# Kernel optimization log

Measured on AMD Instinct MI355X. Metric: run time of the kernel, lower is better.

Reference implementation:

```python
import jax, jax.numpy as jnp
import numpy as np
import math

B, S, D, H = 4, 2048, 1024, 16
DH = D // H
NEG = -1e10


def setup_inputs() -> dict:
    key = jax.random.key(0)
    k1, k2, k3 = jax.random.split(key, 3)
    x = jax.random.normal(k1, (B, S, D), dtype=jnp.float32)
    # torch nn.Linear weights have shape (out_features, in_features); y = x @ W.T + b
    w1 = jax.random.normal(k2, (3 * D, D), dtype=jnp.float32) * (1.0 / math.sqrt(D))
    b1 = jnp.zeros((3 * D,), dtype=jnp.float32)
    w2 = jax.random.normal(k3, (D, D), dtype=jnp.float32) * (1.0 / math.sqrt(D))
    b2 = jnp.zeros((D,), dtype=jnp.float32)
    return {"x": x, "w1": w1, "b1": b1, "w2": w2, "b2": b2}


def reference(x, w1, b1, w2, b2):
    b, s, d = x.shape
    h, dh = H, d // H
    qkv = x @ w1.T + b1                                  # [B,S,3D]
    q, k, v = jnp.split(qkv, 3, axis=-1)                 # each [B,S,D]
    def heads(t):
        return t.reshape(b, s, h, dh).transpose(0, 2, 1, 3)  # [B,H,S,dh]
    q, k, v = heads(q), heads(k), heads(v)
    # additive causal mask: (1 - tril) * -1e10, as in the original
    mask = (1.0 - jnp.tril(jnp.ones((s, s), dtype=x.dtype))) * NEG
    scores = jnp.einsum('bhqd,bhkd->bhqk', q, k) / math.sqrt(dh) + mask
    attn = jax.nn.softmax(scores, axis=-1)
    o = jnp.einsum('bhqk,bhkd->bhqd', attn, v)           # [B,H,S,dh]
    o = o.transpose(0, 2, 1, 3).reshape(b, s, d)         # [B,S,D]
    return o @ w2.T + b2
```

## Files before the change

kernel.cpp:

```cpp
#include <hip/hip_runtime.h>
#include <stdint.h>


typedef __bf16 bf16;
typedef __attribute__((ext_vector_type(4))) __bf16 bf16x4;
typedef __attribute__((ext_vector_type(8))) __bf16 bf16x8;
typedef __attribute__((ext_vector_type(4))) float f32x4;
typedef __attribute__((ext_vector_type(16))) float f32x16;

#define MFMA16(a, b, c) __builtin_amdgcn_mfma_f32_16x16x32_bf16((a), (b), (c), 0, 0, 0)
#define MFMA32(a, b, c) __builtin_amdgcn_mfma_f32_32x32x16_bf16((a), (b), (c), 0, 0, 0)

#if __has_builtin(__builtin_amdgcn_exp2f)
#define EXP2F(x) __builtin_amdgcn_exp2f(x)
#else
#define EXP2F(x) exp2f(x)
#endif

#define GLOAD_LDS16(gp, lp)                                                    \
  __builtin_amdgcn_global_load_lds(                                            \
      (__attribute__((address_space(1))) void*)(gp),                           \
      (__attribute__((address_space(3))) void*)(lp), 16, 0, 0)

#define SB   2048
#define D3   3072
#define DD   1024
#define QSCALE 0.18033688011112042f

__global__ __launch_bounds__(256) void cast_bf16_kernel(
    const float* __restrict__ in, bf16* __restrict__ out, int n4) {
  int stride = gridDim.x * blockDim.x;
  for (int i = blockIdx.x * blockDim.x + threadIdx.x; i < n4; i += stride) {
    float4 v = ((const float4*)in)[i];
    bf16x4 p;
    p[0] = (bf16)v.x; p[1] = (bf16)v.y; p[2] = (bf16)v.z; p[3] = (bf16)v.w;
    *(bf16x4*)(out + (size_t)i * 4) = p;
  }
}

template <int OUTMODE>
__global__ __launch_bounds__(256, 2) void gemm2p_kernel(
    const bf16* __restrict__ A, const bf16* __restrict__ Bw,
    const float* __restrict__ bias, void* __restrict__ Cout,
    int M, int N, int K, int NBn) {
  __shared__ __attribute__((aligned(16))) bf16 As[2][128 * 64];
  __shared__ __attribute__((aligned(16))) bf16 Bs[2][128 * 64];
  const int tid = threadIdx.x;
  const int w = tid >> 6, l = tid & 63;
  const int lr = l & 31, lh = l >> 5;
  const int wm = w >> 1, wn = w & 1;
  const int nwg = gridDim.x;
  const int sw = ((int)blockIdx.x % 8) * (nwg / 8) + (int)blockIdx.x / 8;
  const int bn = sw % NBn, bm = sw / NBn;
  const int m0 = bm * 128, n0 = bn * 128;
  const int NT = K >> 6;

  const int srow = l >> 3;
  const int scol = ((l & 7) ^ srow) << 3;

  auto stage = [&](int buf, int kt) {
#pragma unroll
    for (int j = 0; j < 4; ++j) {
      const int rb = j * 32 + w * 8 + srow;
      GLOAD_LDS16(A + (size_t)(m0 + rb) * K + kt * 64 + scol,
                  (char*)&As[buf][0] + j * 4096 + w * 1024);
      GLOAD_LDS16(Bw + (size_t)(n0 + rb) * K + kt * 64 + scol,
                  (char*)&Bs[buf][0] + j * 4096 + w * 1024);
    }
  };

  auto ldA = [&](int buf, int ks, bf16x8 (&aF)[2]) {
#pragma unroll
    for (int ti = 0; ti < 2; ++ti) {
      const int r = wm * 64 + ti * 32 + lr;
      aF[ti] = *(const bf16x8*)((const char*)&As[buf][0] + r * 128 +
                                (((ks * 2 + lh) ^ (lr & 7)) << 4));
    }
  };
  auto ldB = [&](int buf, int ks, bf16x8 (&bF)[2]) {
#pragma unroll
    for (int tj = 0; tj < 2; ++tj) {
      const int r = wn * 64 + tj * 32 + lr;
      bF[tj] = *(const bf16x8*)((const char*)&Bs[buf][0] + r * 128 +
                                (((ks * 2 + lh) ^ (lr & 7)) << 4));
    }
  };

  f32x16 acc[2][2] = {};
  auto domfma = [&](bf16x8 (&aF)[2], bf16x8 (&bF)[2]) {
    __builtin_amdgcn_s_setprio(1);
#pragma unroll
    for (int ti = 0; ti < 2; ++ti)
#pragma unroll
      for (int tj = 0; tj < 2; ++tj)
        acc[ti][tj] = MFMA32(aF[ti], bF[tj], acc[ti][tj]);
    __builtin_amdgcn_s_setprio(0);
  };

  stage(0, 0);
  __syncthreads();

  for (int T = 0; T < NT; ++T) {
    const int buf = T & 1;
    if (T + 1 < NT) stage(buf ^ 1, T + 1);
    bf16x8 aP[2], bP[2], aQ[2], bQ[2];
    ldA(buf, 0, aP); ldB(buf, 0, bP);
    ldA(buf, 1, aQ); ldB(buf, 1, bQ); domfma(aP, bP);
    ldA(buf, 2, aP); ldB(buf, 2, bP); domfma(aQ, bQ);
    ldA(buf, 3, aQ); ldB(buf, 3, bQ); domfma(aP, bP);
    domfma(aQ, bQ);
    __syncthreads();
  }

#pragma unroll
  for (int ti = 0; ti < 2; ++ti) {
    const int r0 = m0 + wm * 64 + ti * 32 + 4 * lh;
#pragma unroll
    for (int tj = 0; tj < 2; ++tj) {
      const int col = n0 + wn * 64 + tj * 32 + lr;
      const float bv = bias[col];
#pragma unroll
      for (int e = 0; e < 16; ++e) {
        const int row = r0 + (e & 3) + 8 * (e >> 2);
        float v = acc[ti][tj][e] + bv;
        if (OUTMODE == 1) {
          if (col < DD) v *= QSCALE;
          ((bf16*)Cout)[(size_t)row * N + col] = (bf16)v;
        } else {
          ((float*)Cout)[(size_t)row * N + col] = v;
        }
      }
    }
  }
}

__global__ __launch_bounds__(256) void vtrans_kernel(
    const bf16* __restrict__ qkv, bf16* __restrict__ vT) {
  __shared__ __attribute__((aligned(16))) bf16 tt[64 * 72];
  const int tid = threadIdx.x;
  const int bh = blockIdx.x >> 5, st = blockIdx.x & 31;
  const int b = bh >> 4, h = bh & 15;
  const int s0 = st * 64;
  const int sr = tid >> 3, c0 = (tid & 7) * 8;
#pragma unroll
  for (int i = 0; i < 2; ++i) {
    const int srr = sr + i * 32;
    bf16x8 v = *(const bf16x8*)(qkv + (size_t)(b * SB + s0 + srr) * D3 + 2 * DD + h * 64 + c0);
    *(bf16x8*)(&tt[srr * 72 + c0]) = v;
  }
  __syncthreads();
  const int d = tid >> 2;
#pragma unroll
  for (int i = 0; i < 2; ++i) {
    const int sc = (tid & 3) * 2 + i;
    bf16x8 v;
#pragma unroll
    for (int j = 0; j < 8; ++j) v[j] = tt[(sc * 8 + j) * 72 + d];
    *(bf16x8*)(vT + (size_t)(bh * 64 + d) * SB + s0 + sc * 8) = v;
  }
}

__global__ __launch_bounds__(256, 2) void attn_kernel(
    const bf16* __restrict__ qkv, const bf16* __restrict__ vT,
    bf16* __restrict__ o) {
  __shared__ __attribute__((aligned(16))) bf16 Kt[2][128 * 64];
  __shared__ __attribute__((aligned(16))) bf16 Vt[2][64 * 128];
  const int tid = threadIdx.x;
  const int w = tid >> 6, l = tid & 63;
  const int c = l & 15, g = l >> 4;
  const int pair = blockIdx.x >> 6, bh = blockIdx.x & 63;
  const int b = bh >> 4, h = bh & 15;
  const int qtA = pair, qtB = 15 - pair;
  const int swz = (c & 7) << 4;

  const bf16* qg = qkv + (size_t)(b * SB) * D3 + h * 64;

  auto stage = [&](int kt, int buf) {
#pragma unroll
    for (int j = 0; j < 4; ++j) {
      const int row = w * 32 + j * 8 + (l >> 3);
      const int cs = ((l & 7) ^ (row & 7)) << 3;
      GLOAD_LDS16(qkv + (size_t)(b * SB + kt * 128 + row) * D3 + DD + h * 64 + cs,
                  (char*)&Kt[buf][0] + w * 4096 + j * 1024);
    }
#pragma unroll
    for (int j = 0; j < 4; ++j) {
      const int row = w * 16 + j * 4 + (l >> 4);
      const int cs = ((l & 15) ^ (row & 7)) << 3;
      GLOAD_LDS16(vT + (size_t)(bh * 64 + row) * SB + kt * 128 + cs,
                  (char*)&Vt[buf][0] + w * 4096 + j * 1024);
    }
  };

  stage(0, 0);

  bf16x8 qfA[2][2], qfB[2][2];
#pragma unroll
  for (int mi = 0; mi < 2; ++mi)
#pragma unroll
    for (int dk = 0; dk < 2; ++dk) {
      qfA[mi][dk] = *(const bf16x8*)(qg + (size_t)(qtA * 128 + w * 32 + mi * 16 + c) * D3 + dk * 32 + g * 8);
      qfB[mi][dk] = *(const bf16x8*)(qg + (size_t)(qtB * 128 + w * 32 + mi * 16 + c) * D3 + dk * 32 + g * 8);
    }

  f32x4 ofA[2][4] = {}, ofB[2][4] = {};
  float mA[2] = {-1e30f, -1e30f}, lA[2] = {0.f, 0.f};
  float mB[2] = {-1e30f, -1e30f}, lB[2] = {0.f, 0.f};
  const f32x4 zero = {0.f, 0.f, 0.f, 0.f};

  auto process = [&](int kt, int qt, int buf, bf16x8 (&qf)[2][2], float (&m)[2],
                     float (&lsum)[2], f32x4 (&of)[2][4]) {
    f32x4 sf[2][8];
#pragma unroll
    for (int f = 0; f < 8; ++f) {
      const char* kr = (const char*)&Kt[buf][0] + (f * 16 + c) * 128;
      bf16x8 kb0 = *(const bf16x8*)(kr + ((g * 16) ^ swz));
      bf16x8 kb1 = *(const bf16x8*)(kr + ((64 + g * 16) ^ swz));
#pragma unroll
      for (int mi = 0; mi < 2; ++mi) {
        f32x4 t = MFMA16(kb0, qf[mi][0], zero);
        sf[mi][f] = MFMA16(kb1, qf[mi][1], t);
      }
    }

    if (kt == qt) {
#pragma unroll
      for (int mi = 0; mi < 2; ++mi) {
        const int qloc = w * 32 + mi * 16 + c;
#pragma unroll
        for (int f = 0; f < 8; ++f)
#pragma unroll
          for (int r = 0; r < 4; ++r)
            if (f * 16 + 4 * g + r > qloc) sf[mi][f][r] = -1e30f;
      }
    }

    bf16x8 pa[2][4];
#pragma unroll
    for (int mi = 0; mi < 2; ++mi) {
      float pm = -1e30f;
#pragma unroll
      for (int f = 0; f < 8; ++f)
#pragma unroll
        for (int r = 0; r < 4; ++r) pm = fmaxf(pm, sf[mi][f][r]);
      pm = fmaxf(pm, __shfl_xor(pm, 16, 64));
      pm = fmaxf(pm, __shfl_xor(pm, 32, 64));
      if (__any(pm > m[mi] + 8.f)) {
        const float mnew = fmaxf(m[mi], pm);
        const float sc = EXP2F(m[mi] - mnew);
        m[mi] = mnew;
        lsum[mi] *= sc;
#pragma unroll
        for (int di = 0; di < 4; ++di) of[mi][di] *= sc;
      }
      float rs = 0.f;
#pragma unroll
      for (int f = 0; f < 8; ++f)
#pragma unroll
        for (int r = 0; r < 4; ++r) {
          const float pv = EXP2F(sf[mi][f][r] - m[mi]);
          sf[mi][f][r] = pv;
          rs += pv;
        }
      rs += __shfl_xor(rs, 16, 64);
      rs += __shfl_xor(rs, 32, 64);
      lsum[mi] += rs;
#pragma unroll
      for (int t = 0; t < 4; ++t)
#pragma unroll
        for (int s = 0; s < 4; ++s) {
          pa[mi][t][s]     = (bf16)sf[mi][2 * t][s];
          pa[mi][t][4 + s] = (bf16)sf[mi][2 * t + 1][s];
        }
    }

#pragma unroll
    for (int di = 0; di < 4; ++di) {
      const char* vrow = (const char*)&Vt[buf][0] + (di * 16 + c) * 256;
#pragma unroll
      for (int t = 0; t < 4; ++t) {
        bf16x4 v1 = *(const bf16x4*)(vrow + ((64 * t + 8 * g) ^ swz));
        bf16x4 v2 = *(const bf16x4*)(vrow + ((64 * t + 32 + 8 * g) ^ swz));
        bf16x8 va;
#pragma unroll
        for (int s = 0; s < 4; ++s) { va[s] = v1[s]; va[4 + s] = v2[s]; }
#pragma unroll
        for (int mi = 0; mi < 2; ++mi)
          of[mi][di] = MFMA16(va, pa[mi][t], of[mi][di]);
      }
    }
  };

  __syncthreads();

  int buf = 0;
  for (int kt = 0; kt <= qtB; ++kt) {
    if (kt < qtB) stage(kt + 1, buf ^ 1);
    if (kt <= qtA) process(kt, qtA, buf, qfA, mA, lA, ofA);
    process(kt, qtB, buf, qfB, mB, lB, ofB);
    __syncthreads();
    buf ^= 1;
  }

  auto store_tile = [&](int qt, float (&lsum)[2], f32x4 (&of)[2][4]) {
#pragma unroll
    for (int mi = 0; mi < 2; ++mi) {
      const float inv = 1.0f / lsum[mi];
      const size_t row = (size_t)(b * SB + qt * 128 + w * 32 + mi * 16 + c);
#pragma unroll
      for (int di = 0; di < 4; ++di) {
        bf16x4 st;
#pragma unroll
        for (int r = 0; r < 4; ++r) st[r] = (bf16)(of[mi][di][r] * inv);
        *(bf16x4*)(o + row * DD + h * 64 + di * 16 + 4 * g) = st;
      }
    }
  };
  store_tile(qtA, lA, ofA);
  store_tile(qtB, lB, ofB);
}

extern "C" void kernel_launch(void* const* d_in, const int* in_sizes, int n_in,
                              void* d_out, int out_size, void* d_ws, size_t ws_size,
                              hipStream_t stream) {
  const float* x  = (const float*)d_in[0];
  const float* w1 = (const float*)d_in[1];
  const float* b1 = (const float*)d_in[2];
  const float* w2 = (const float*)d_in[3];
  const float* b2 = (const float*)d_in[4];
  float* out = (float*)d_out;

  bf16* xb   = (bf16*)d_ws;
  bf16* w1b  = xb   + (size_t)8  * 1024 * 1024;
  bf16* w2b  = w1b  + (size_t)3  * 1024 * 1024;
  bf16* qkvb = w2b  + (size_t)1  * 1024 * 1024;
  bf16* vT   = qkvb + (size_t)8192 * 3072;
  bf16* ob   = vT   + (size_t)8  * 1024 * 1024;

  cast_bf16_kernel<<<2048, 256, 0, stream>>>(x,  xb,  (8 * 1024 * 1024) / 4);
  cast_bf16_kernel<<<768,  256, 0, stream>>>(w1, w1b, (3 * 1024 * 1024) / 4);
  cast_bf16_kernel<<<256,  256, 0, stream>>>(w2, w2b, (1 * 1024 * 1024) / 4);

  gemm2p_kernel<1><<<1536, 256, 0, stream>>>(xb, w1b, b1, qkvb, 8192, 3072, 1024, 24);
  vtrans_kernel<<<2048, 256, 0, stream>>>(qkvb, vT);
  attn_kernel<<<512, 256, 0, stream>>>(qkvb, vT, ob);
  gemm2p_kernel<0><<<512, 256, 0, stream>>>(ob, w2b, b2, out, 8192, 1024, 1024, 8);
}
```

Before: 174.8 us.

## Enlarge GEMM tiles to 512-thread blocks with templated per-wave fragments

Generalizes the GEMM kernel into a template with per-wave fragment counts FM and FN and moves it to 8 waves per block. The QKV projection now uses 256x256 tiles over 384 blocks, and the output projection uses 128x256 tiles over 256 blocks. Larger tiles raise arithmetic intensity and cut global and LDS traffic per FLOP. In exchange there are more accumulator registers and only one block per CU, so less latency hiding, and the smaller grids may leave part of the GPU idle.

```diff
diff --git a/kernel.cpp b/kernel.cpp
--- a/kernel.cpp
+++ b/kernel.cpp
@@ -38,21 +38,22 @@
   }
 }
 
-template <int OUTMODE>
-__global__ __launch_bounds__(256, 2) void gemm2p_kernel(
+template <int OUTMODE, int FM, int FN>
+__global__ __launch_bounds__(512, 1) void gemmks_kernel(
     const bf16* __restrict__ A, const bf16* __restrict__ Bw,
     const float* __restrict__ bias, void* __restrict__ Cout,
     int M, int N, int K, int NBn) {
-  __shared__ __attribute__((aligned(16))) bf16 As[2][128 * 64];
-  __shared__ __attribute__((aligned(16))) bf16 Bs[2][128 * 64];
+  constexpr int BM = FM * 64, BN = FN * 128;
+  __shared__ __attribute__((aligned(16))) bf16 As[2][BM * 64];
+  __shared__ __attribute__((aligned(16))) bf16 Bs[2][BN * 64];
   const int tid = threadIdx.x;
   const int w = tid >> 6, l = tid & 63;
   const int lr = l & 31, lh = l >> 5;
-  const int wm = w >> 1, wn = w & 1;
+  const int wm = w >> 2, wn = w & 3;
   const int nwg = gridDim.x;
   const int sw = ((int)blockIdx.x % 8) * (nwg / 8) + (int)blockIdx.x / 8;
   const int bn = sw % NBn, bm = sw / NBn;
-  const int m0 = bm * 128, n0 = bn * 128;
+  const int m0 = bm * BM, n0 = bn * BN;
   const int NT = K >> 6;
 
   const int srow = l >> 3;
@@ -60,39 +61,43 @@
 
   auto stage = [&](int buf, int kt) {
 #pragma unroll
-    for (int j = 0; j < 4; ++j) {
-      const int rb = j * 32 + w * 8 + srow;
+    for (int j = 0; j < FM; ++j) {
+      const int rb = j * 64 + w * 8 + srow;
       GLOAD_LDS16(A + (size_t)(m0 + rb) * K + kt * 64 + scol,
-                  (char*)&As[buf][0] + j * 4096 + w * 1024);
+                  (char*)&As[buf][0] + j * 8192 + w * 1024);
+    }
+#pragma unroll
+    for (int j = 0; j < 2 * FN; ++j) {
+      const int rb = j * 64 + w * 8 + srow;
       GLOAD_LDS16(Bw + (size_t)(n0 + rb) * K + kt * 64 + scol,
-                  (char*)&Bs[buf][0] + j * 4096 + w * 1024);
-    }
-  };
-
-  auto ldA = [&](int buf, int ks, bf16x8 (&aF)[2]) {
-#pragma unroll
-    for (int ti = 0; ti < 2; ++ti) {
-      const int r = wm * 64 + ti * 32 + lr;
+                  (char*)&Bs[buf][0] + j * 8192 + w * 1024);
+    }
+  };
+
+  auto ldA = [&](int buf, int ks, bf16x8 (&aF)[FM]) {
+#pragma unroll
+    for (int ti = 0; ti < FM; ++ti) {
+      const int r = wm * (FM * 32) + ti * 32 + lr;
       aF[ti] = *(const bf16x8*)((const char*)&As[buf][0] + r * 128 +
                                 (((ks * 2 + lh) ^ (lr & 7)) << 4));
     }
   };
-  auto ldB = [&](int buf, int ks, bf16x8 (&bF)[2]) {
-#pragma unroll
-    for (int tj = 0; tj < 2; ++tj) {
-      const int r = wn * 64 + tj * 32 + lr;
+  auto ldB = [&](int buf, int ks, bf16x8 (&bF)[FN]) {
+#pragma unroll
+    for (int tj = 0; tj < FN; ++tj) {
+      const int r = wn * (FN * 32) + tj * 32 + lr;
       bF[tj] = *(const bf16x8*)((const char*)&Bs[buf][0] + r * 128 +
                                 (((ks * 2 + lh) ^ (lr & 7)) << 4));
     }
   };
 
-  f32x16 acc[2][2] = {};
-  auto domfma = [&](bf16x8 (&aF)[2], bf16x8 (&bF)[2]) {
+  f32x16 acc[FM][FN] = {};
+  auto domfma = [&](bf16x8 (&aF)[FM], bf16x8 (&bF)[FN]) {
     __builtin_amdgcn_s_setprio(1);
 #pragma unroll
-    for (int ti = 0; ti < 2; ++ti)
-#pragma unroll
-      for (int tj = 0; tj < 2; ++tj)
+    for (int ti = 0; ti < FM; ++ti)
+#pragma unroll
+      for (int tj = 0; tj < FN; ++tj)
         acc[ti][tj] = MFMA32(aF[ti], bF[tj], acc[ti][tj]);
     __builtin_amdgcn_s_setprio(0);
   };
@@ -103,7 +108,7 @@
   for (int T = 0; T < NT; ++T) {
     const int buf = T & 1;
     if (T + 1 < NT) stage(buf ^ 1, T + 1);
-    bf16x8 aP[2], bP[2], aQ[2], bQ[2];
+    bf16x8 aP[FM], bP[FN], aQ[FM], bQ[FN];
     ldA(buf, 0, aP); ldB(buf, 0, bP);
     ldA(buf, 1, aQ); ldB(buf, 1, bQ); domfma(aP, bP);
     ldA(buf, 2, aP); ldB(buf, 2, bP); domfma(aQ, bQ);
@@ -113,11 +118,11 @@
   }
 
 #pragma unroll
-  for (int ti = 0; ti < 2; ++ti) {
-    const int r0 = m0 + wm * 64 + ti * 32 + 4 * lh;
-#pragma unroll
-    for (int tj = 0; tj < 2; ++tj) {
-      const int col = n0 + wn * 64 + tj * 32 + lr;
+  for (int ti = 0; ti < FM; ++ti) {
+    const int r0 = m0 + wm * (FM * 32) + ti * 32 + 4 * lh;
+#pragma unroll
+    for (int tj = 0; tj < FN; ++tj) {
+      const int col = n0 + wn * (FN * 32) + tj * 32 + lr;
       const float bv = bias[col];
 #pragma unroll
       for (int e = 0; e < 16; ++e) {
@@ -341,8 +346,8 @@
   cast_bf16_kernel<<<768,  256, 0, stream>>>(w1, w1b, (3 * 1024 * 1024) / 4);
   cast_bf16_kernel<<<256,  256, 0, stream>>>(w2, w2b, (1 * 1024 * 1024) / 4);
 
-  gemm2p_kernel<1><<<1536, 256, 0, stream>>>(xb, w1b, b1, qkvb, 8192, 3072, 1024, 24);
+  gemmks_kernel<1, 4, 2><<<384, 512, 0, stream>>>(xb, w1b, b1, qkvb, 8192, 3072, 1024, 12);
   vtrans_kernel<<<2048, 256, 0, stream>>>(qkvb, vT);
   attn_kernel<<<512, 256, 0, stream>>>(qkvb, vT, ob);
-  gemm2p_kernel<0><<<512, 256, 0, stream>>>(ob, w2b, b2, out, 8192, 1024, 1024, 8);
-}
+  gemmks_kernel<0, 2, 2><<<256, 512, 0, stream>>>(ob, w2b, b2, out, 8192, 1024, 1024, 4);
+}
```

Result: slower. 179.1 us (+2.5%).
